# Kernel optimization log

Hardware: AMD Instinct MI355X
Metric: run time of the kernel (lower is better)

Reference implementation:

```python
import math
import jax, jax.numpy as jnp
import numpy as np

N_STEPS = 4

def rotate_half(x):
    h = x.shape[-1] // 2
    return jnp.concatenate([-x[..., h:], x[..., :h]], axis=-1)

def setup_inputs() -> dict:
    key = jax.random.key(0)
    k0, k1, k2, k3 = jax.random.split(key, 4)
    B, N, F, D = 2, 4096, 512, 64
    features = jax.random.normal(k0, (B, N, F), jnp.float32)
    # standard RoPE tables, shape [N, D]
    inv_freq = 1.0 / (10000.0 ** (jnp.arange(0, D, 2, dtype=jnp.float32) / D))
    ang = jnp.arange(N, dtype=jnp.float32)[:, None] * inv_freq[None, :]  # [N, D/2]
    ang = jnp.concatenate([ang, ang], axis=-1)  # [N, D]
    cos, sin = jnp.cos(ang), jnp.sin(ang)
    # causal mask broadcast to [B, N, N]
    mask = jnp.broadcast_to(jnp.tril(jnp.ones((N, N), bool)), (B, N, N))
    s = 1.0 / math.sqrt(F)
    Wq = jax.random.normal(k1, (F, D), jnp.float32) * s
    Wk = jax.random.normal(k2, (F, D), jnp.float32) * s
    charge_w = jax.random.normal(k3, (F, 1), jnp.float32) * s
    charge_b = jnp.zeros((1,), jnp.float32)
    step_size = jnp.full((1,), 0.5, jnp.float32)
    charge_decay = jnp.full((1,), 0.3, jnp.float32)
    return dict(features=features, cos=cos, sin=sin, mask=mask, Wq=Wq, Wk=Wk,
                charge_w=charge_w, charge_b=charge_b,
                step_size=step_size, charge_decay=charge_decay)

def reference(features, cos, sin, mask, Wq, Wk, charge_w, charge_b, step_size, charge_decay):
    d_k = Wq.shape[-1]
    Q = jnp.einsum('bnf,fd->bnd', features, Wq)
    K = jnp.einsum('bnf,fd->bnd', features, Wk)
    c, s = cos[None, :, :], sin[None, :, :]  # broadcast over batch
    Q = Q * c + rotate_half(Q) * s
    K = K * c + rotate_half(K) * s
    compat = jnp.einsum('bnd,bmd->bnm', Q, K) / math.sqrt(d_k)  # [B,N,N]
    charge = jax.nn.sigmoid(jnp.einsum('bnf,fo->bno', features, charge_w)[..., 0] + charge_b[0])  # [B,N]
    neg_inf = jnp.asarray(-jnp.inf, compat.dtype)
    logits = jnp.where(mask, compat, neg_inf)
    ss = step_size[0]
    cd = charge_decay[0]
    for _ in range(N_STEPS):
        attn = jax.nn.softmax(logits, axis=-1)
        received = attn.sum(axis=-2)  # column sums, [B,N]
        charge = charge * (1.0 - cd * jax.nn.sigmoid(received - 1.0))
        energy = -compat * charge[..., :, None] * charge[..., None, :]
        logits = jnp.where(mask, logits - ss * energy, neg_inf)
    return jax.nn.softmax(logits, axis=-1)
```

## Files before the change

kernel.cpp:

```cpp
#include <hip/hip_runtime.h>
#include <math.h>

#define NTOK   4096
#define NFEAT  512
#define NDIM   64
#define RROWS  8
#define NBANDS (NTOK / RROWS)

__device__ __forceinline__ float block_max256(float v, float* s) {
#pragma unroll
  for (int o = 32; o > 0; o >>= 1) v = fmaxf(v, __shfl_down(v, o, 64));
  int tid = threadIdx.x;
  if ((tid & 63) == 0) s[tid >> 6] = v;
  __syncthreads();
  v = fmaxf(fmaxf(s[0], s[1]), fmaxf(s[2], s[3]));
  __syncthreads();
  return v;
}
__device__ __forceinline__ float block_sum256(float v, float* s) {
#pragma unroll
  for (int o = 32; o > 0; o >>= 1) v += __shfl_down(v, o, 64);
  int tid = threadIdx.x;
  if ((tid & 63) == 0) s[tid >> 6] = v;
  __syncthreads();
  v = s[0] + s[1] + s[2] + s[3];
  __syncthreads();
  return v;
}

__global__ __launch_bounds__(256) void qk_kernel(
    const float* __restrict__ feat, const float* __restrict__ cosb,
    const float* __restrict__ sinb, const float* __restrict__ Wq,
    const float* __restrict__ Wk, const float* __restrict__ cw,
    const float* __restrict__ cbp, float* __restrict__ Q, float* __restrict__ K,
    float* __restrict__ cur, float* __restrict__ chist)
{
  __shared__ __align__(16) float smem[RROWS * NFEAT];
  const int tid  = threadIdx.x;
  const int row0 = blockIdx.x * RROWS;

  const float4* fb4 = (const float4*)(feat + (size_t)row0 * NFEAT);
  float4* sm4 = (float4*)smem;
#pragma unroll
  for (int i = tid; i < RROWS * NFEAT / 4; i += 256) sm4[i] = fb4[i];
  if (tid < RROWS * 4) chist[row0 * 4 + tid] = 0.f;
  __syncthreads();

  const int r   = tid >> 5;
  const int c   = tid & 31;
  const int isQ = (c < 16);
  const int d0  = (c & 15) * 4;
  const float* __restrict__ Wp = isQ ? Wq : Wk;
  const float* fr = smem + (r << 9);

  float a0 = 0.f, a1 = 0.f, a2 = 0.f, a3 = 0.f;
  for (int k = 0; k < NFEAT; ++k) {
    float fv = fr[k];
    float4 w = *(const float4*)(Wp + k * NDIM + d0);
    a0 = fmaf(fv, w.x, a0); a1 = fmaf(fv, w.y, a1);
    a2 = fmaf(fv, w.z, a2); a3 = fmaf(fv, w.w, a3);
  }

  float accc = 0.f;
#pragma unroll
  for (int j = 0; j < 16; ++j) accc = fmaf(fr[c + (j << 5)], cw[c + (j << 5)], accc);
#pragma unroll
  for (int o = 16; o > 0; o >>= 1) accc += __shfl_down(accc, o, 64);
  if (c == 0) {
    float cb = cbp[0];
    cur[row0 + r] = 1.f / (1.f + __expf(-(accc + cb)));
  }
  __syncthreads();

  float* sraw = smem;
  {
    float* dst = sraw + r * 132 + (isQ ? 0 : 64) + d0;
    dst[0] = a0; dst[1] = a1; dst[2] = a2; dst[3] = a3;
  }
  __syncthreads();

#pragma unroll
  for (int i = tid; i < RROWS * NDIM; i += 256) {
    int rr = i >> 6, d = i & 63;
    int g = row0 + rr, n = g & (NTOK - 1);
    float cv = cosb[(n << 6) + d], sv = sinb[(n << 6) + d];
    float qv = sraw[rr * 132 + d];
    float qr = (d < 32) ? -sraw[rr * 132 + d + 32] : sraw[rr * 132 + d - 32];
    Q[(size_t)g * NDIM + d] = qv * cv + qr * sv;
    float kv = sraw[rr * 132 + 64 + d];
    float kr = (d < 32) ? -sraw[rr * 132 + 64 + d + 32] : sraw[rr * 132 + 64 + d - 32];
    K[(size_t)g * NDIM + d] = kv * cv + kr * sv;
  }
}

__global__ __launch_bounds__(256) void compat_kernel(
    const float* __restrict__ Q, const float* __restrict__ K, float* __restrict__ C)
{
  __shared__ __align__(16) float Qs[32][132];
  __shared__ __align__(16) float Ks[32][132];
  int p = blockIdx.x, b = 0;
  if (p >= 528) { b = 1; p -= 528; }
  int ti = (int)((sqrtf(8.f * p + 1.f) - 1.f) * 0.5f);
  while ((ti + 1) * (ti + 2) / 2 <= p) ++ti;
  while (ti * (ti + 1) / 2 > p) --ti;
  int tj = p - ti * (ti + 1) / 2;

  const int tid = threadIdx.x;
  const int ty = tid >> 4, tx = tid & 15;
  const int i0 = ty * 8, j0 = tx * 8;
  const size_t qbase = ((size_t)b * NTOK + (size_t)ti * 128) * NDIM;
  const size_t kbase = ((size_t)b * NTOK + (size_t)tj * 128) * NDIM;

  float acc[8][8];
#pragma unroll
  for (int ii = 0; ii < 8; ++ii)
#pragma unroll
    for (int jj = 0; jj < 8; ++jj) acc[ii][jj] = 0.f;

  for (int dk = 0; dk < NDIM; dk += 32) {
    __syncthreads();
    for (int i = tid; i < 128 * 32; i += 256) {
      int row = i >> 5, d = i & 31;
      Qs[d][row] = Q[qbase + (size_t)row * NDIM + dk + d];
      Ks[d][row] = K[kbase + (size_t)row * NDIM + dk + d];
    }
    __syncthreads();
#pragma unroll
    for (int d = 0; d < 32; ++d) {
      float4 q0 = *(const float4*)&Qs[d][i0];
      float4 q1 = *(const float4*)&Qs[d][i0 + 4];
      float4 k0 = *(const float4*)&Ks[d][j0];
      float4 k1 = *(const float4*)&Ks[d][j0 + 4];
      float av[8] = {q0.x, q0.y, q0.z, q0.w, q1.x, q1.y, q1.z, q1.w};
      float bv[8] = {k0.x, k0.y, k0.z, k0.w, k1.x, k1.y, k1.z, k1.w};
#pragma unroll
      for (int ii = 0; ii < 8; ++ii)
#pragma unroll
        for (int jj = 0; jj < 8; ++jj)
          acc[ii][jj] = fmaf(av[ii], bv[jj], acc[ii][jj]);
    }
  }
#pragma unroll
  for (int ii = 0; ii < 8; ++ii) {
    size_t grow = (size_t)b * NTOK + (size_t)ti * 128 + i0 + ii;
    float4 w0 = make_float4(acc[ii][0] * 0.125f, acc[ii][1] * 0.125f,
                            acc[ii][2] * 0.125f, acc[ii][3] * 0.125f);
    float4 w1 = make_float4(acc[ii][4] * 0.125f, acc[ii][5] * 0.125f,
                            acc[ii][6] * 0.125f, acc[ii][7] * 0.125f);
    *(float4*)&C[grow * NTOK + (size_t)tj * 128 + j0]     = w0;
    *(float4*)&C[grow * NTOK + (size_t)tj * 128 + j0 + 4] = w1;
  }
}

template <int MODE>
__global__ __launch_bounds__(256) void pass_kernel(
    const float* __restrict__ compat, const float4* __restrict__ chist,
    const float* __restrict__ ssp, float* __restrict__ partial,
    float* __restrict__ out)
{
  __shared__ float sred[4];
  const int tid = threadIdx.x;
  int band = blockIdx.x, b = 0;
  if (band >= NBANDS) { b = 1; band -= NBANDS; }
  const int n0 = band * RROWS;
  const int kmax = (n0 + RROWS - 1) >> 8;
  const float ss = ssp[0];

  float4 ch[16];
#pragma unroll
  for (int k = 0; k < 16; ++k)
    if (k <= kmax) ch[k] = chist[(b << 12) + tid + (k << 8)];

  float cs[16];
#pragma unroll
  for (int k = 0; k < 16; ++k) cs[k] = 0.f;

  for (int rr = 0; rr < RROWS; ++rr) {
    const int n = n0 + rr;
    const float* rowp = compat + ((size_t)((b << 12) + n) << 12);
    float4 h = chist[(b << 12) + n];
    h.x *= ss; h.y *= ss; h.z *= ss; h.w *= ss;

    float e[16];
    float vmax = -INFINITY;
#pragma unroll
    for (int k = 0; k < 16; ++k) {
      if (k > kmax) continue;
      const int col = tid + (k << 8);
      float x = -INFINITY;
      if (col <= n) {
        float cv  = rowp[col];
        float dot = fmaf(ch[k].x, h.x,
                    fmaf(ch[k].y, h.y, fmaf(ch[k].z, h.z, ch[k].w * h.w)));
        x = fmaf(cv, dot, cv);
      }
      e[k] = x;
      vmax = fmaxf(vmax, x);
    }
    float M = block_max256(vmax, sred);
    float lsum = 0.f;
#pragma unroll
    for (int k = 0; k < 16; ++k) {
      if (k > kmax) continue;
      float v = __expf(e[k] - M);
      e[k] = v;
      lsum += v;
    }
    float L = block_sum256(lsum, sred);
    float inv = 1.f / L;
    if (MODE == 0) {
#pragma unroll
      for (int k = 0; k < 16; ++k)
        if (k <= kmax) cs[k] += e[k] * inv;
    } else {
      float* orow = out + ((size_t)((b << 12) + n) << 12);
#pragma unroll
      for (int k = 0; k < 16; ++k) {
        if (k <= kmax) orow[tid + (k << 8)] = e[k] * inv;
        else           orow[tid + (k << 8)] = 0.f;
      }
    }
  }
  if (MODE == 0) {
    float* pp = partial + ((size_t)b * NBANDS + band) * NTOK;
    const int cmax = n0 + RROWS - 1;
#pragma unroll
    for (int k = 0; k < 16; ++k) {
      if (k > kmax) continue;
      int col = tid + (k << 8);
      if (col <= cmax) pp[col] = cs[k];
    }
  }
}

__global__ __launch_bounds__(256) void reduce_update_kernel(
    const float* __restrict__ partial, const float* __restrict__ cdp,
    float* __restrict__ cur, float* __restrict__ chist, int step)
{
  __shared__ float s[8][32];
  const int tid = threadIdx.x;
  const int b = blockIdx.x >> 7;
  const int m0 = (blockIdx.x & 127) << 5;
  const int ml = tid & 31, seg = tid >> 5;
  const int m = m0 + ml;
  const int bmin = m >> 3;
  float sum = 0.f;
  const float* pb = partial + (size_t)b * NBANDS * NTOK + m;
  for (int band = bmin + seg; band < NBANDS; band += 8)
    sum += pb[(size_t)band << 12];
  s[seg][ml] = sum;
  __syncthreads();
  if (seg == 0) {
    float r = s[0][ml] + s[1][ml] + s[2][ml] + s[3][ml] +
              s[4][ml] + s[5][ml] + s[6][ml] + s[7][ml];
    float sg = 1.f / (1.f + __expf(-(r - 1.f)));
    float cd = cdp[0];
    int idx = (b << 12) + m;
    float c = cur[idx] * (1.f - cd * sg);
    cur[idx] = c;
    chist[idx * 4 + step] = c;
  }
}

extern "C" void kernel_launch(void* const* d_in, const int* in_sizes, int n_in,
                              void* d_out, int out_size, void* d_ws, size_t ws_size,
                              hipStream_t stream) {
  const float* feat = (const float*)d_in[0];
  const float* cosb = (const float*)d_in[1];
  const float* sinb = (const float*)d_in[2];
  const float* Wq  = (const float*)d_in[4];
  const float* Wk  = (const float*)d_in[5];
  const float* cw  = (const float*)d_in[6];
  const float* cbp = (const float*)d_in[7];
  const float* ssp = (const float*)d_in[8];
  const float* cdp = (const float*)d_in[9];
  float* out = (float*)d_out;

  float* ws      = (float*)d_ws;
  float* Q       = ws;
  float* K       = ws + 524288;
  float* chist   = ws + 1048576;
  float* cur     = ws + 1081344;
  float* partial = ws + 1089536;

  qk_kernel<<<1024, 256, 0, stream>>>(feat, cosb, sinb, Wq, Wk, cw, cbp, Q, K, cur, chist);
  compat_kernel<<<1056, 256, 0, stream>>>(Q, K, out);
  for (int t = 0; t < 4; ++t) {
    pass_kernel<0><<<2 * NBANDS, 256, 0, stream>>>(out, (const float4*)chist, ssp, partial, nullptr);
    reduce_update_kernel<<<256, 256, 0, stream>>>(partial, cdp, cur, chist, t);
  }
  pass_kernel<1><<<2 * NBANDS, 256, 0, stream>>>(out, (const float4*)chist, ssp, nullptr, out);
}
```

Measured before the change: 735.8 us.

## Assign one wavefront per row with paired causal rows and LDS atomic column sums

Reworks the softmax pass kernel so that each 64-lane wavefront owns a whole row, and each block processes a short row together with its mirrored long row for causal load balance. Reductions become wave-level shuffles with no block barriers. In MODE 0, column sums are accumulated through LDS atomics into a full-width per-block partial, and the reduce kernel's band range is adjusted to match the new layout. The cost is a 64-entry register array per thread, higher register pressure and LDS atomic contention, and full 4096-wide partial writes per block.

Measured after the change: 992.2 us. +34.9%, slower.

```diff
diff --git a/kernel.cpp b/kernel.cpp
--- a/kernel.cpp
+++ b/kernel.cpp
@@ -5,28 +5,7 @@
 #define NFEAT  512
 #define NDIM   64
 #define RROWS  8
-#define NBANDS (NTOK / RROWS)
-
-__device__ __forceinline__ float block_max256(float v, float* s) {
-#pragma unroll
-  for (int o = 32; o > 0; o >>= 1) v = fmaxf(v, __shfl_down(v, o, 64));
-  int tid = threadIdx.x;
-  if ((tid & 63) == 0) s[tid >> 6] = v;
-  __syncthreads();
-  v = fmaxf(fmaxf(s[0], s[1]), fmaxf(s[2], s[3]));
-  __syncthreads();
-  return v;
-}
-__device__ __forceinline__ float block_sum256(float v, float* s) {
-#pragma unroll
-  for (int o = 32; o > 0; o >>= 1) v += __shfl_down(v, o, 64);
-  int tid = threadIdx.x;
-  if ((tid & 63) == 0) s[tid >> 6] = v;
-  __syncthreads();
-  v = s[0] + s[1] + s[2] + s[3];
-  __syncthreads();
-  return v;
-}
+#define NBANDS 512
 
 __global__ __launch_bounds__(256) void qk_kernel(
     const float* __restrict__ feat, const float* __restrict__ cosb,
@@ -158,78 +137,95 @@
     const float* __restrict__ ssp, float* __restrict__ partial,
     float* __restrict__ out)
 {
-  __shared__ float sred[4];
+  __shared__ float rp[NTOK];
   const int tid = threadIdx.x;
-  int band = blockIdx.x, b = 0;
-  if (band >= NBANDS) { b = 1; band -= NBANDS; }
-  const int n0 = band * RROWS;
-  const int kmax = (n0 + RROWS - 1) >> 8;
+  int p = blockIdx.x, b = 0;
+  if (p >= NBANDS) { b = 1; p -= NBANDS; }
+  const int w = tid >> 6;
+  const int l = tid & 63;
   const float ss = ssp[0];
-
-  float4 ch[16];
-#pragma unroll
-  for (int k = 0; k < 16; ++k)
-    if (k <= kmax) ch[k] = chist[(b << 12) + tid + (k << 8)];
-
-  float cs[16];
-#pragma unroll
-  for (int k = 0; k < 16; ++k) cs[k] = 0.f;
-
-  for (int rr = 0; rr < RROWS; ++rr) {
-    const int n = n0 + rr;
-    const float* rowp = compat + ((size_t)((b << 12) + n) << 12);
-    float4 h = chist[(b << 12) + n];
+  const float4* __restrict__ chb = chist + (b << 12);
+
+  if (MODE == 0) {
+    for (int i = tid; i < NTOK; i += 256) rp[i] = 0.f;
+    __syncthreads();
+  }
+
+  for (int half = 0; half < 2; ++half) {
+    const int n = half ? (NTOK - 1 - ((p << 2) + w)) : ((p << 2) + w);
+    const int K = n >> 6;
+    const float* __restrict__ rowp = compat + ((size_t)((b << 12) + n) << 12);
+    float4 h = chb[n];
     h.x *= ss; h.y *= ss; h.z *= ss; h.w *= ss;
 
-    float e[16];
+    float e[64];
     float vmax = -INFINITY;
 #pragma unroll
-    for (int k = 0; k < 16; ++k) {
-      if (k > kmax) continue;
-      const int col = tid + (k << 8);
-      float x = -INFINITY;
-      if (col <= n) {
-        float cv  = rowp[col];
-        float dot = fmaf(ch[k].x, h.x,
-                    fmaf(ch[k].y, h.y, fmaf(ch[k].z, h.z, ch[k].w * h.w)));
-        x = fmaf(cv, dot, cv);
-      }
-      e[k] = x;
-      vmax = fmaxf(vmax, x);
-    }
-    float M = block_max256(vmax, sred);
-    float lsum = 0.f;
-#pragma unroll
-    for (int k = 0; k < 16; ++k) {
-      if (k > kmax) continue;
-      float v = __expf(e[k] - M);
-      e[k] = v;
-      lsum += v;
-    }
-    float L = block_sum256(lsum, sred);
-    float inv = 1.f / L;
+    for (int c0 = 0; c0 < 64; c0 += 4) {
+      if (c0 > K) continue;
+      float  cv[4];
+      float4 c4[4];
+#pragma unroll
+      for (int i = 0; i < 4; ++i) {
+        const int col = ((c0 + i) << 6) + l;
+        cv[i] = rowp[col];
+        c4[i] = chb[col];
+      }
+#pragma unroll
+      for (int i = 0; i < 4; ++i) {
+        const int col = ((c0 + i) << 6) + l;
+        float dot = fmaf(c4[i].x, h.x,
+                    fmaf(c4[i].y, h.y, fmaf(c4[i].z, h.z, c4[i].w * h.w)));
+        float x = fmaf(cv[i], dot, cv[i]);
+        x = (col <= n) ? x : -INFINITY;
+        e[c0 + i] = x;
+        vmax = fmaxf(vmax, x);
+      }
+    }
+#pragma unroll
+    for (int o = 32; o > 0; o >>= 1) vmax = fmaxf(vmax, __shfl_xor(vmax, o, 64));
+
+    float s = 0.f;
+#pragma unroll
+    for (int c0 = 0; c0 < 64; c0 += 4) {
+      if (c0 > K) continue;
+#pragma unroll
+      for (int i = 0; i < 4; ++i) {
+        float v = __expf(e[c0 + i] - vmax);
+        e[c0 + i] = v;
+        s += v;
+      }
+    }
+#pragma unroll
+    for (int o = 32; o > 0; o >>= 1) s += __shfl_xor(s, o, 64);
+    const float inv = 1.f / s;
+
     if (MODE == 0) {
 #pragma unroll
-      for (int k = 0; k < 16; ++k)
-        if (k <= kmax) cs[k] += e[k] * inv;
+      for (int c0 = 0; c0 < 64; c0 += 4) {
+        if (c0 > K) continue;
+#pragma unroll
+        for (int i = 0; i < 4; ++i)
+          atomicAdd(&rp[((c0 + i) << 6) + l], e[c0 + i] * inv);
+      }
     } else {
-      float* orow = out + ((size_t)((b << 12) + n) << 12);
-#pragma unroll
-      for (int k = 0; k < 16; ++k) {
-        if (k <= kmax) orow[tid + (k << 8)] = e[k] * inv;
-        else           orow[tid + (k << 8)] = 0.f;
-      }
-    }
-  }
+      float* __restrict__ orow = out + ((size_t)((b << 12) + n) << 12);
+#pragma unroll
+      for (int c0 = 0; c0 < 64; c0 += 4) {
+        const bool act = (c0 <= K);
+#pragma unroll
+        for (int i = 0; i < 4; ++i) {
+          const int col = ((c0 + i) << 6) + l;
+          orow[col] = act ? e[c0 + i] * inv : 0.f;
+        }
+      }
+    }
+  }
+
   if (MODE == 0) {
-    float* pp = partial + ((size_t)b * NBANDS + band) * NTOK;
-    const int cmax = n0 + RROWS - 1;
-#pragma unroll
-    for (int k = 0; k < 16; ++k) {
-      if (k > kmax) continue;
-      int col = tid + (k << 8);
-      if (col <= cmax) pp[col] = cs[k];
-    }
+    __syncthreads();
+    float* __restrict__ pp = partial + ((size_t)b * NBANDS + p) * (size_t)NTOK;
+    for (int i = tid; i < NTOK; i += 256) pp[i] = rp[i];
   }
 }
 
@@ -243,10 +239,11 @@
   const int m0 = (blockIdx.x & 127) << 5;
   const int ml = tid & 31, seg = tid >> 5;
   const int m = m0 + ml;
-  const int bmin = m >> 3;
+  int pmax = (NTOK - 1 - m) >> 2;
+  if (pmax > NBANDS - 1) pmax = NBANDS - 1;
   float sum = 0.f;
   const float* pb = partial + (size_t)b * NBANDS * NTOK + m;
-  for (int band = bmin + seg; band < NBANDS; band += 8)
+  for (int band = seg; band <= pmax; band += 8)
     sum += pb[(size_t)band << 12];
   s[seg][ml] = sum;
   __syncthreads();
```
